# Kernel tuning notes

Measured on AMD Instinct MI355X. Metric: run time of the kernel, lower is better.

## Reference

```python
import jax, jax.numpy as jnp
import numpy as np

NUM_CLASSES = 80
POSITIVE_OVERLAP = 0.5
NEGATIVE_OVERLAP = 0.4
BBOX_STD = 0.2  # keras-retinanet default bbox_transform std (mean=0)


def _make_boxes(key, shape, img_size=800.0, max_wh=120.0):
    """Build valid (x1,y1,x2,y2) boxes with x2>x1, y2>y1."""
    k1, k2 = jax.random.split(key)
    xy1 = jax.random.uniform(k1, shape[:-1] + (2,)) * (img_size - max_wh)
    wh = jax.random.uniform(k2, shape[:-1] + (2,)) * (max_wh - 4.0) + 4.0
    return jnp.concatenate([xy1, xy1 + wh], axis=-1)


def setup_inputs() -> dict:
    key = jax.random.key(0)
    ka, kl, kan = jax.random.split(key, 3)
    B, N, A = 8, 64, 120000
    gt_boxes = _make_boxes(ka, (B, N, 4))  # [B,N,4]
    labels = jax.random.randint(kl, (B, N), 0, NUM_CLASSES).astype(jnp.float32)
    annotations_batch = jnp.concatenate([gt_boxes, labels[..., None]], axis=-1)  # [B,N,5]
    anchors = _make_boxes(kan, (A, 4))  # [A,4]
    return {"annotations_batch": annotations_batch, "anchors": anchors}


def _compute_iou(anchors, boxes):
    # anchors [A,4], boxes [N,4] -> IoU [A,N]
    iw = jnp.minimum(anchors[:, None, 2], boxes[None, :, 2]) - jnp.maximum(anchors[:, None, 0], boxes[None, :, 0])
    ih = jnp.minimum(anchors[:, None, 3], boxes[None, :, 3]) - jnp.maximum(anchors[:, None, 1], boxes[None, :, 1])
    inter = jnp.maximum(iw, 0.0) * jnp.maximum(ih, 0.0)
    area_a = ((anchors[:, 2] - anchors[:, 0]) * (anchors[:, 3] - anchors[:, 1]))[:, None]
    area_b = ((boxes[:, 2] - boxes[:, 0]) * (boxes[:, 3] - boxes[:, 1]))[None, :]
    union = jnp.maximum(area_a + area_b - inter, 1e-8)
    return inter / union


def _targets_single(annotations, anchors):
    # annotations [N,5], anchors [A,4]
    boxes = annotations[:, :4]
    labels = annotations[:, 4].astype(jnp.int32)

    overlaps = _compute_iou(anchors, boxes)          # [A,N]
    argmax_inds = jnp.argmax(overlaps, axis=1)       # [A]
    max_overlaps = jnp.max(overlaps, axis=1)         # [A]

    positive = max_overlaps >= POSITIVE_OVERLAP
    ignore = (max_overlaps > NEGATIVE_OVERLAP) & (~positive)
    anchor_states = jnp.where(positive, 1.0, jnp.where(ignore, -1.0, 0.0))  # [A]

    # classification target: one-hot label of best gt, only for positives
    cls_target = jax.nn.one_hot(labels[argmax_inds], NUM_CLASSES, dtype=boxes.dtype)
    cls_target = cls_target * positive[:, None].astype(boxes.dtype)         # [A,C]

    # bbox target = gt box of best-overlap annotation, then bbox_transform
    bbox_target = boxes[argmax_inds]                 # [A,4]
    aw = anchors[:, 2] - anchors[:, 0]
    ah = anchors[:, 3] - anchors[:, 1]
    reg_target = jnp.stack([
        (bbox_target[:, 0] - anchors[:, 0]) / aw,
        (bbox_target[:, 1] - anchors[:, 1]) / ah,
        (bbox_target[:, 2] - anchors[:, 2]) / aw,
        (bbox_target[:, 3] - anchors[:, 3]) / ah,
    ], axis=1) / BBOX_STD                            # [A,4]

    return cls_target, reg_target, anchor_states


def reference(annotations_batch, anchors):
    # vmap over the image/batch dim; anchors shared
    cls_b, reg_b, states_b = jax.vmap(_targets_single, in_axes=(0, None))(annotations_batch, anchors)
    return cls_b, reg_b, states_b
```

## Files before the change

### kernel.cpp

```cpp
#include <hip/hip_runtime.h>

#define NUM_CLASSES 80

__global__ __launch_bounds__(256) void targets_kernel(
    const float* __restrict__ ann, const float* __restrict__ anchors,
    float* __restrict__ cls, float* __restrict__ reg, float* __restrict__ states,
    int A, int N) {
#pragma clang fp contract(off)
  __shared__ float4 sbox[64];
  __shared__ float sarea[64];
  __shared__ int slabel[64];
  __shared__ int sinfo[256];

  const int b = blockIdx.y;
  const int a0 = blockIdx.x * 256;
  const int tid = threadIdx.x;

  if (tid < N) {
    const float* p = ann + ((size_t)b * N + tid) * 5;
    float x1 = p[0], y1 = p[1], x2 = p[2], y2 = p[3];
    sbox[tid] = make_float4(x1, y1, x2, y2);
    sarea[tid] = (x2 - x1) * (y2 - y1);
    slabel[tid] = (int)p[4];
  }
  __syncthreads();

  const int a = a0 + tid;
  const bool valid = (a < A);
  const int aidx = valid ? a : 0;
  const float4 anc = reinterpret_cast<const float4*>(anchors)[aidx];
  const float area_a = (anc.z - anc.x) * (anc.w - anc.y);

  float best_inter, best_uni;
  {
    float4 bx = sbox[0];
    float iw = fminf(anc.z, bx.z) - fmaxf(anc.x, bx.x);
    float ih = fminf(anc.w, bx.w) - fmaxf(anc.y, bx.y);
    best_inter = fmaxf(iw, 0.0f) * fmaxf(ih, 0.0f);
    best_uni = fmaxf(area_a + sarea[0] - best_inter, 1e-8f);
  }
  int bestj = 0;
  #pragma unroll 16
  for (int j = 1; j < N; ++j) {
    float4 bx = sbox[j];
    float iw = fminf(anc.z, bx.z) - fmaxf(anc.x, bx.x);
    float ih = fminf(anc.w, bx.w) - fmaxf(anc.y, bx.y);
    float inter = fmaxf(iw, 0.0f) * fmaxf(ih, 0.0f);
    float uni = fmaxf(area_a + sarea[j] - inter, 1e-8f);
    bool upd = (inter * best_uni) > (best_inter * uni);
    best_inter = upd ? inter : best_inter;
    best_uni = upd ? uni : best_uni;
    bestj = upd ? j : bestj;
  }
  const float best = best_inter / best_uni;

  const bool positive = best >= 0.5f;
  const bool ignore = (best > 0.4f) && !positive;
  const float state = positive ? 1.0f : (ignore ? -1.0f : 0.0f);

  if (valid) {
    float4 bt = sbox[bestj];
    float aw = anc.z - anc.x;
    float ah = anc.w - anc.y;
    float4 r;
    r.x = ((bt.x - anc.x) / aw) / 0.2f;
    r.y = ((bt.y - anc.y) / ah) / 0.2f;
    r.z = ((bt.z - anc.z) / aw) / 0.2f;
    r.w = ((bt.w - anc.w) / ah) / 0.2f;
    reinterpret_cast<float4*>(reg)[(size_t)b * A + a] = r;
    states[(size_t)b * A + a] = state;
  }
  sinfo[tid] = positive ? slabel[bestj] : -1;
  const int npos = __syncthreads_count(positive && valid);

  const int nvalid = min(256, A - a0);
  float4* clsv = reinterpret_cast<float4*>(cls + ((size_t)b * A + a0) * NUM_CLASSES);
  const int total = nvalid * (NUM_CLASSES / 4);
  if (npos == 0) {
    const float4 z = make_float4(0.0f, 0.0f, 0.0f, 0.0f);
    for (int it = tid; it < total; it += 256) clsv[it] = z;
  } else {
    for (int it = tid; it < total; it += 256) {
      int al = it / (NUM_CLASSES / 4);
      int w = it - al * (NUM_CLASSES / 4);
      int lab = sinfo[al];
      int c0 = w * 4;
      float4 v;
      v.x = (lab == c0 + 0) ? 1.0f : 0.0f;
      v.y = (lab == c0 + 1) ? 1.0f : 0.0f;
      v.z = (lab == c0 + 2) ? 1.0f : 0.0f;
      v.w = (lab == c0 + 3) ? 1.0f : 0.0f;
      clsv[it] = v;
    }
  }
}

extern "C" void kernel_launch(void* const* d_in, const int* in_sizes, int n_in,
                              void* d_out, int out_size, void* d_ws, size_t ws_size,
                              hipStream_t stream) {
  const float* ann = (const float*)d_in[0];
  const float* anchors = (const float*)d_in[1];

  const int A = in_sizes[1] / 4;
  const int B = (int)((long long)out_size / ((long long)A * (NUM_CLASSES + 5)));
  const int N = in_sizes[0] / (B * 5);

  float* out = (float*)d_out;
  float* cls = out;
  float* reg = cls + (size_t)B * A * NUM_CLASSES;
  float* states = reg + (size_t)B * A * 4;

  dim3 grid((A + 255) / 256, B);
  targets_kernel<<<grid, 256, 0, stream>>>(ann, anchors, cls, reg, states, A, N);
}
```

Baseline: 66.14 us.

## Use persistent grid-stride blocks with all batch annotations staged once in shared memory

The launch becomes a fixed grid of 1024 persistent blocks. Each block loads the annotations for every batch image into shared memory once, then loops over (batch, anchor-tile) work items instead of launching one block per tile. This removes the per-block annotation reload and the scheduling cost of roughly 3750 blocks. In exchange it adds an extra barrier per tile, uses more LDS (512 boxes, which caps N*B), and limits parallelism to 1024 blocks.

New measurement: 65.93 us. Within noise of the previous version (-0.3%).

```diff
diff --git a/kernel.cpp b/kernel.cpp
--- a/kernel.cpp
+++ b/kernel.cpp
@@ -1,96 +1,105 @@
 #include <hip/hip_runtime.h>
 
 #define NUM_CLASSES 80
+#define NBLK 1024
 
 __global__ __launch_bounds__(256) void targets_kernel(
     const float* __restrict__ ann, const float* __restrict__ anchors,
     float* __restrict__ cls, float* __restrict__ reg, float* __restrict__ states,
-    int A, int N) {
+    int A, int N, int B, int ntiles) {
 #pragma clang fp contract(off)
-  __shared__ float4 sbox[64];
-  __shared__ float sarea[64];
-  __shared__ int slabel[64];
+  __shared__ float4 sbox[512];
+  __shared__ float sarea[512];
+  __shared__ int slabel[512];
   __shared__ int sinfo[256];
 
-  const int b = blockIdx.y;
-  const int a0 = blockIdx.x * 256;
   const int tid = threadIdx.x;
+  const int NB = N * B;
 
-  if (tid < N) {
-    const float* p = ann + ((size_t)b * N + tid) * 5;
+  for (int i = tid; i < NB; i += 256) {
+    const float* p = ann + (size_t)i * 5;
     float x1 = p[0], y1 = p[1], x2 = p[2], y2 = p[3];
-    sbox[tid] = make_float4(x1, y1, x2, y2);
-    sarea[tid] = (x2 - x1) * (y2 - y1);
-    slabel[tid] = (int)p[4];
+    sbox[i] = make_float4(x1, y1, x2, y2);
+    sarea[i] = (x2 - x1) * (y2 - y1);
+    slabel[i] = (int)p[4];
   }
   __syncthreads();
 
-  const int a = a0 + tid;
-  const bool valid = (a < A);
-  const int aidx = valid ? a : 0;
-  const float4 anc = reinterpret_cast<const float4*>(anchors)[aidx];
-  const float area_a = (anc.z - anc.x) * (anc.w - anc.y);
+  const int T = B * ntiles;
+  for (int t = blockIdx.x; t < T; t += NBLK) {
+    const int b = t / ntiles;
+    const int tile = t - b * ntiles;
+    const int a0 = tile * 256;
+    const int a = a0 + tid;
+    const bool valid = (a < A);
+    const int aidx = valid ? a : 0;
+    const float4 anc = reinterpret_cast<const float4*>(anchors)[aidx];
+    const float area_a = (anc.z - anc.x) * (anc.w - anc.y);
+    const int boff = b * N;
 
-  float best_inter, best_uni;
-  {
-    float4 bx = sbox[0];
-    float iw = fminf(anc.z, bx.z) - fmaxf(anc.x, bx.x);
-    float ih = fminf(anc.w, bx.w) - fmaxf(anc.y, bx.y);
-    best_inter = fmaxf(iw, 0.0f) * fmaxf(ih, 0.0f);
-    best_uni = fmaxf(area_a + sarea[0] - best_inter, 1e-8f);
-  }
-  int bestj = 0;
-  #pragma unroll 16
-  for (int j = 1; j < N; ++j) {
-    float4 bx = sbox[j];
-    float iw = fminf(anc.z, bx.z) - fmaxf(anc.x, bx.x);
-    float ih = fminf(anc.w, bx.w) - fmaxf(anc.y, bx.y);
-    float inter = fmaxf(iw, 0.0f) * fmaxf(ih, 0.0f);
-    float uni = fmaxf(area_a + sarea[j] - inter, 1e-8f);
-    bool upd = (inter * best_uni) > (best_inter * uni);
-    best_inter = upd ? inter : best_inter;
-    best_uni = upd ? uni : best_uni;
-    bestj = upd ? j : bestj;
-  }
-  const float best = best_inter / best_uni;
+    float best_inter, best_uni;
+    {
+      float4 bx = sbox[boff];
+      float iw = fminf(anc.z, bx.z) - fmaxf(anc.x, bx.x);
+      float ih = fminf(anc.w, bx.w) - fmaxf(anc.y, bx.y);
+      best_inter = fmaxf(iw, 0.0f) * fmaxf(ih, 0.0f);
+      best_uni = fmaxf(area_a + sarea[boff] - best_inter, 1e-8f);
+    }
+    int bestj = 0;
+    #pragma unroll 8
+    for (int j = 1; j < N; ++j) {
+      float4 bx = sbox[boff + j];
+      float iw = fminf(anc.z, bx.z) - fmaxf(anc.x, bx.x);
+      float ih = fminf(anc.w, bx.w) - fmaxf(anc.y, bx.y);
+      float inter = fmaxf(iw, 0.0f) * fmaxf(ih, 0.0f);
+      float uni = fmaxf(area_a + sarea[boff + j] - inter, 1e-8f);
+      bool upd = (inter * best_uni) > (best_inter * uni);
+      best_inter = upd ? inter : best_inter;
+      best_uni = upd ? uni : best_uni;
+      bestj = upd ? j : bestj;
+    }
+    const float best = best_inter / best_uni;
 
-  const bool positive = best >= 0.5f;
-  const bool ignore = (best > 0.4f) && !positive;
-  const float state = positive ? 1.0f : (ignore ? -1.0f : 0.0f);
+    const bool positive = best >= 0.5f;
+    const bool ignore = (best > 0.4f) && !positive;
+    const float state = positive ? 1.0f : (ignore ? -1.0f : 0.0f);
 
-  if (valid) {
-    float4 bt = sbox[bestj];
-    float aw = anc.z - anc.x;
-    float ah = anc.w - anc.y;
-    float4 r;
-    r.x = ((bt.x - anc.x) / aw) / 0.2f;
-    r.y = ((bt.y - anc.y) / ah) / 0.2f;
-    r.z = ((bt.z - anc.z) / aw) / 0.2f;
-    r.w = ((bt.w - anc.w) / ah) / 0.2f;
-    reinterpret_cast<float4*>(reg)[(size_t)b * A + a] = r;
-    states[(size_t)b * A + a] = state;
-  }
-  sinfo[tid] = positive ? slabel[bestj] : -1;
-  const int npos = __syncthreads_count(positive && valid);
+    if (valid) {
+      float4 bt = sbox[boff + bestj];
+      float aw = anc.z - anc.x;
+      float ah = anc.w - anc.y;
+      float4 r;
+      r.x = ((bt.x - anc.x) / aw) / 0.2f;
+      r.y = ((bt.y - anc.y) / ah) / 0.2f;
+      r.z = ((bt.z - anc.z) / aw) / 0.2f;
+      r.w = ((bt.w - anc.w) / ah) / 0.2f;
+      reinterpret_cast<float4*>(reg)[(size_t)b * A + a] = r;
+      states[(size_t)b * A + a] = state;
+    }
 
-  const int nvalid = min(256, A - a0);
-  float4* clsv = reinterpret_cast<float4*>(cls + ((size_t)b * A + a0) * NUM_CLASSES);
-  const int total = nvalid * (NUM_CLASSES / 4);
-  if (npos == 0) {
-    const float4 z = make_float4(0.0f, 0.0f, 0.0f, 0.0f);
-    for (int it = tid; it < total; it += 256) clsv[it] = z;
-  } else {
-    for (int it = tid; it < total; it += 256) {
-      int al = it / (NUM_CLASSES / 4);
-      int w = it - al * (NUM_CLASSES / 4);
-      int lab = sinfo[al];
-      int c0 = w * 4;
-      float4 v;
-      v.x = (lab == c0 + 0) ? 1.0f : 0.0f;
-      v.y = (lab == c0 + 1) ? 1.0f : 0.0f;
-      v.z = (lab == c0 + 2) ? 1.0f : 0.0f;
-      v.w = (lab == c0 + 3) ? 1.0f : 0.0f;
-      clsv[it] = v;
+    __syncthreads();
+    sinfo[tid] = positive ? slabel[boff + bestj] : -1;
+    const int npos = __syncthreads_count(valid && positive);
+
+    const int nvalid = min(256, A - a0);
+    float4* clsv = reinterpret_cast<float4*>(cls + ((size_t)b * A + a0) * NUM_CLASSES);
+    const int total = nvalid * (NUM_CLASSES / 4);
+    if (npos == 0) {
+      const float4 z = make_float4(0.0f, 0.0f, 0.0f, 0.0f);
+      for (int it = tid; it < total; it += 256) clsv[it] = z;
+    } else {
+      for (int it = tid; it < total; it += 256) {
+        int al = it / (NUM_CLASSES / 4);
+        int w = it - al * (NUM_CLASSES / 4);
+        int lab = sinfo[al];
+        int c0 = w * 4;
+        float4 v;
+        v.x = (lab == c0 + 0) ? 1.0f : 0.0f;
+        v.y = (lab == c0 + 1) ? 1.0f : 0.0f;
+        v.z = (lab == c0 + 2) ? 1.0f : 0.0f;
+        v.w = (lab == c0 + 3) ? 1.0f : 0.0f;
+        clsv[it] = v;
+      }
     }
   }
 }
@@ -104,12 +113,12 @@
   const int A = in_sizes[1] / 4;
   const int B = (int)((long long)out_size / ((long long)A * (NUM_CLASSES + 5)));
   const int N = in_sizes[0] / (B * 5);
+  const int ntiles = (A + 255) / 256;
 
   float* out = (float*)d_out;
   float* cls = out;
   float* reg = cls + (size_t)B * A * NUM_CLASSES;
   float* states = reg + (size_t)B * A * 4;
 
-  dim3 grid((A + 255) / 256, B);
-  targets_kernel<<<grid, 256, 0, stream>>>(ann, anchors, cls, reg, states, A, N);
+  targets_kernel<<<NBLK, 256, 0, stream>>>(ann, anchors, cls, reg, states, A, N, B, ntiles);
 }
```
